# Optimization experiments

Measured on AMD Instinct MI355X. Metric: run time of the kernel, lower is better.

Reference implementation:

```python
import jax, jax.numpy as jnp
import numpy as np


def setup_inputs() -> dict:
    key = jax.random.key(0)
    kx, ky = jax.random.split(key)
    x = jax.random.normal(kx, (4, 8192, 3), dtype=jnp.float32)
    y = jax.random.normal(ky, (4, 8192, 3), dtype=jnp.float32)
    return {"x": x, "y": y}


def _chamfer(x, y):
    # x: [B, N, D], y: [B, M, D]
    x2 = jnp.sum(x * x, axis=-1)                      # [B, N]
    y2 = jnp.sum(y * y, axis=-1)                      # [B, M]
    xy = jnp.einsum("bnd,bmd->bnm", x, y)             # [B, N, M]
    d2 = x2[:, :, None] + y2[:, None, :] - 2.0 * xy   # [B, N, M]
    d2 = jnp.maximum(d2, 0.0)
    cham_x = jnp.min(d2, axis=2).mean(axis=1)         # [B] min over M, mean over N
    cham_y = jnp.min(d2, axis=1).mean(axis=1)         # [B] min over N, mean over M
    return cham_x + cham_y                            # [B]


def reference(x, y):
    per_batch = _chamfer(x, y)
    return jnp.mean(per_batch)  # batch_reduction='mean'
```

## Files before the change

### kernel.cpp

```cpp
#include <hip/hip_runtime.h>


#define N_      8192
#define RPB     4096
#define NRECS   16384
#define NQ      65536
#define FLT_BIG 3.0e38f

typedef float v2f  __attribute__((ext_vector_type(2)));
typedef unsigned int v16u __attribute__((ext_vector_type(16)));

__global__ void zero_out_kernel(float* out) { *out = 0.0f; }

__global__ __launch_bounds__(256) void prep_kernel(
    const float* __restrict__ x, const float* __restrict__ y,
    float4* __restrict__ xrec, float4* __restrict__ yrec,
    unsigned int* __restrict__ pmin, float* __restrict__ out)
{
    int i = blockIdx.x * 256 + threadIdx.x;
    if (i == 0) *out = 0.0f;
    pmin[i]         = 0x7F800000u;
    pmin[i + 32768] = 0x7F800000u;
    int side = i >> 14;
    int r    = i & (NRECS - 1);
    const float* src = side ? y : x;
    float4*      dst = side ? yrec : xrec;
    const float* p = src + (size_t)r * 6;
    float p0x = p[0], p0y = p[1], p0z = p[2];
    float p1x = p[3], p1y = p[4], p1z = p[5];
    float w0 = fmaf(p0x, p0x, fmaf(p0y, p0y, p0z * p0z));
    float w1 = fmaf(p1x, p1x, fmaf(p1y, p1y, p1z * p1z));
    dst[2*r]   = make_float4(p0x, p1x, p0y, p1y);
    dst[2*r+1] = make_float4(p0z, p1z, w0, w1);
}


static __device__ __forceinline__ void s_load2(v16u& a, v16u& b, const unsigned int* p) {
    asm volatile("s_load_dwordx16 %0, %2, 0x0\n\t"
                 "s_load_dwordx16 %1, %2, 0x40"
                 : "=s"(a), "=s"(b) : "s"(p));
}
static __device__ __forceinline__ void s_wait(v16u& a, v16u& b) {
    asm volatile("s_waitcnt lgkmcnt(0)" : "+s"(a), "+s"(b));
}

static __device__ __forceinline__ void do_record(
    const unsigned int* d,
    const v2f* qx, const v2f* qy, const v2f* qz,
    float* acc)
{
    v2f pxs = (v2f){__uint_as_float(d[0]), __uint_as_float(d[1])};
    v2f pys = (v2f){__uint_as_float(d[2]), __uint_as_float(d[3])};
    v2f pzs = (v2f){__uint_as_float(d[4]), __uint_as_float(d[5])};
    v2f w2v = (v2f){__uint_as_float(d[6]), __uint_as_float(d[7])};
    #pragma unroll
    for (int j = 0; j < 4; ++j) {
        v2f td, ts;
        asm("v_pk_fma_f32 %0, %1, %2, %3"
            : "=v"(td) : "v"(qz[j]), "s"(pzs), "v"(w2v));
        asm("v_pk_fma_f32 %0, %1, %2, %3 op_sel:[0,1,1] op_sel_hi:[1,0,0]"
            : "=v"(ts) : "v"(qz[j]), "s"(pzs), "v"(w2v));
        asm("v_pk_fma_f32 %0, %1, %2, %0"
            : "+v"(td) : "v"(qy[j]), "s"(pys));
        asm("v_pk_fma_f32 %0, %1, %2, %0 op_sel:[0,1,0] op_sel_hi:[1,0,1]"
            : "+v"(ts) : "v"(qy[j]), "s"(pys));
        asm("v_pk_fma_f32 %0, %1, %2, %0"
            : "+v"(td) : "v"(qx[j]), "s"(pxs));
        asm("v_pk_fma_f32 %0, %1, %2, %0 op_sel:[0,1,0] op_sel_hi:[1,0,1]"
            : "+v"(ts) : "v"(qx[j]), "s"(pxs));
        asm("v_min3_f32 %0, %0, %1, %2" : "+v"(acc[2*j])   : "v"(td.x), "v"(ts.x));
        asm("v_min3_f32 %0, %0, %1, %2" : "+v"(acc[2*j+1]) : "v"(td.y), "v"(ts.y));
    }
}

__global__ __launch_bounds__(512, 4) void chamfer_kernel(
    const float* __restrict__ xraw, const float* __restrict__ yraw,
    const float4* __restrict__ xrec, const float4* __restrict__ yrec,
    unsigned int* __restrict__ pmin)
{
    __shared__ float red[8 * 512];

    const int tid  = threadIdx.x;
    const int lane = tid & 63;
    const int wave = __builtin_amdgcn_readfirstlane(tid >> 6);
    const int blk  = blockIdx.x;
    const int dir   = blk >> 8;
    const int batch = (blk >> 6) & 3;
    const int qg    = (blk >> 2) & 15;
    const int seg   = blk & 3;

    const float*  qraw = dir ? yraw : xraw;
    const float4* orec = dir ? xrec : yrec;

    const int qbase = batch * N_ + qg * 512;
    float f[24];
    {
        const float4* qv = (const float4*)(qraw + (size_t)qbase * 3) + lane * 6;
        #pragma unroll
        for (int k = 0; k < 6; ++k) {
            float4 t = qv[k];
            f[4*k] = t.x; f[4*k+1] = t.y; f[4*k+2] = t.z; f[4*k+3] = t.w;
        }
    }
    v2f qx[4], qy[4], qz[4];
    float acc[8];
    #pragma unroll
    for (int j = 0; j < 4; ++j) {
        qx[j] = (v2f){-2.0f * f[6*j+0], -2.0f * f[6*j+3]};
        qy[j] = (v2f){-2.0f * f[6*j+1], -2.0f * f[6*j+4]};
        qz[j] = (v2f){-2.0f * f[6*j+2], -2.0f * f[6*j+5]};
        acc[2*j] = FLT_BIG; acc[2*j+1] = FLT_BIG;
    }

    const unsigned int* sp = (const unsigned int*)
        (orec + (size_t)2 * (batch * RPB + seg * 1024 + wave * 128));
    v16u a0, a1, b0, b1;
    s_load2(a0, a1, sp);
    for (int g = 0; g < 32; g += 2) {
        s_wait(a0, a1);
        if (g + 1 < 32) s_load2(b0, b1, sp + (g + 1) * 32);
        {
            unsigned int da[16], db[16];
            #pragma unroll
            for (int t = 0; t < 16; ++t) { da[t] = a0[t]; db[t] = a1[t]; }
            do_record(da,     qx, qy, qz, acc);
            do_record(da + 8, qx, qy, qz, acc);
            do_record(db,     qx, qy, qz, acc);
            do_record(db + 8, qx, qy, qz, acc);
        }
        s_wait(b0, b1);
        if (g + 2 < 32) s_load2(a0, a1, sp + (g + 2) * 32);
        {
            unsigned int da[16], db[16];
            #pragma unroll
            for (int t = 0; t < 16; ++t) { da[t] = b0[t]; db[t] = b1[t]; }
            do_record(da,     qx, qy, qz, acc);
            do_record(da + 8, qx, qy, qz, acc);
            do_record(db,     qx, qy, qz, acc);
            do_record(db + 8, qx, qy, qz, acc);
        }
    }

    #pragma unroll
    for (int j = 0; j < 8; ++j) red[wave * 512 + lane * 8 + j] = acc[j];
    __syncthreads();

    float m = red[tid];
    #pragma unroll
    for (int w = 1; w < 8; ++w) m = fminf(m, red[w * 512 + tid]);
    int gq = qbase + tid;
    float ax = qraw[gq*3+0], ay = qraw[gq*3+1], az = qraw[gq*3+2];
    float qn = fmaf(ax, ax, fmaf(ay, ay, az * az));
    float d2 = fmaxf(0.0f, qn + m);
    atomicMin(&pmin[dir * 32768 + gq], __float_as_uint(d2));
}

__global__ __launch_bounds__(256) void sum_kernel(
    const unsigned int* __restrict__ pmin, float* __restrict__ out)
{
    int i = blockIdx.x * 256 + threadIdx.x;
    float4 v = ((const float4*)pmin)[i];
    float s = v.x + v.y + v.z + v.w;
    #pragma unroll
    for (int off = 32; off > 0; off >>= 1) s += __shfl_xor(s, off);
    if ((threadIdx.x & 63) == 0) atomicAdd(out, s * (1.0f / 32768.0f));
}

__global__ __launch_bounds__(1024) void chamfer_raw_kernel(
    const float* __restrict__ xraw, const float* __restrict__ yraw,
    float* __restrict__ out)
{
    __shared__ float4 red4[16][64];
    const int tid  = threadIdx.x;
    const int wave = tid >> 6;
    const int lane = tid & 63;
    const int blk  = blockIdx.x;
    const bool xdir = (blk < 128);
    const int b    = (blk & 127) >> 5;
    const int qofs = (blk & 31) << 8;
    const float* qraw = xdir ? xraw : yraw;
    const float* oraw = xdir ? yraw : xraw;
    float qx0[4], qx1[4], qx2[4], acc[4];
    #pragma unroll
    for (int q = 0; q < 4; ++q) {
        int gq = b * N_ + qofs + lane*4 + q;
        qx0[q] = qraw[gq*3+0]; qx1[q] = qraw[gq*3+1]; qx2[q] = qraw[gq*3+2];
        acc[q] = FLT_BIG;
    }
    const float* opp = oraw + (size_t)(b * N_ + wave * 512) * 3;
    #pragma unroll 4
    for (int k = 0; k < 512; ++k) {
        float p0 = opp[k*3+0], p1 = opp[k*3+1], p2 = opp[k*3+2];
        float w  = fmaf(p0, p0, fmaf(p1, p1, p2*p2));
        #pragma unroll
        for (int q = 0; q < 4; ++q) {
            float dot = qx0[q]*p0 + qx1[q]*p1 + qx2[q]*p2;
            acc[q] = fminf(acc[q], fmaf(-2.0f, dot, w));
        }
    }
    red4[wave][lane] = make_float4(acc[0], acc[1], acc[2], acc[3]);
    __syncthreads();
    if (tid < 256) {
        const float* red = (const float*)red4;
        float m = red[tid];
        #pragma unroll
        for (int w = 1; w < 16; ++w) m = fminf(m, red[w*256 + tid]);
        int gq = b * N_ + qofs + tid;
        float ax = qraw[gq*3+0], ay = qraw[gq*3+1], az = qraw[gq*3+2];
        float d2 = fmaxf(0.0f, fmaf(ax,ax,fmaf(ay,ay,az*az)) + m);
        #pragma unroll
        for (int off = 32; off > 0; off >>= 1) d2 += __shfl_xor(d2, off);
        if ((tid & 63) == 0) atomicAdd(out, d2 * (1.0f / 32768.0f));
    }
}

extern "C" void kernel_launch(void* const* d_in, const int* in_sizes, int n_in,
                              void* d_out, int out_size, void* d_ws, size_t ws_size,
                              hipStream_t stream)
{
    const float* x = (const float*)d_in[0];
    const float* y = (const float*)d_in[1];
    float* out = (float*)d_out;

    const size_t need = (size_t)NRECS * 2 * 2 * sizeof(float4) + NQ * 4;
    if (ws_size >= need) {
        float4* xrec = (float4*)d_ws;
        float4* yrec = xrec + 2 * NRECS;
        unsigned int* pmin = (unsigned int*)(yrec + 2 * NRECS);
        prep_kernel<<<128, 256, 0, stream>>>(x, y, xrec, yrec, pmin, out);
        chamfer_kernel<<<512, 512, 0, stream>>>(x, y, xrec, yrec, pmin);
        sum_kernel<<<64, 256, 0, stream>>>(pmin, out);
    } else {
        zero_out_kernel<<<1, 1, 0, stream>>>(out);
        chamfer_raw_kernel<<<256, 1024, 0, stream>>>(x, y, out);
    }
}
```

Baseline: 98.04 us.

## Fuse prep and sum into chamfer kernel with LDS records and last-block reduction

Removes the separate prep and sum kernels. Each block now builds its packed opposite-point records, including squared norms, directly in LDS, and reads them from LDS instead of through scalar loads. The cross-segment min goes through a workspace partial buffer plus an atomic counter, and the last-arriving block per group finishes the min and sum. A global counter then writes the final output. This saves launch overhead and global round-trips, but adds a memset, threadfence ordering, and LDS reads in the inner loop, which replace the earlier SGPR operands.

New measurement: 105.6 us. +7.7%, slower.

```diff
diff --git a/kernel.cpp b/kernel.cpp
--- a/kernel.cpp
+++ b/kernel.cpp
@@ -2,72 +2,33 @@
 
 
 #define N_      8192
-#define RPB     4096
-#define NRECS   16384
-#define NQ      65536
+#define NGRP    128
 #define FLT_BIG 3.0e38f
 
-typedef float v2f  __attribute__((ext_vector_type(2)));
-typedef unsigned int v16u __attribute__((ext_vector_type(16)));
+typedef float v2f __attribute__((ext_vector_type(2)));
 
 __global__ void zero_out_kernel(float* out) { *out = 0.0f; }
 
-__global__ __launch_bounds__(256) void prep_kernel(
-    const float* __restrict__ x, const float* __restrict__ y,
-    float4* __restrict__ xrec, float4* __restrict__ yrec,
-    unsigned int* __restrict__ pmin, float* __restrict__ out)
-{
-    int i = blockIdx.x * 256 + threadIdx.x;
-    if (i == 0) *out = 0.0f;
-    pmin[i]         = 0x7F800000u;
-    pmin[i + 32768] = 0x7F800000u;
-    int side = i >> 14;
-    int r    = i & (NRECS - 1);
-    const float* src = side ? y : x;
-    float4*      dst = side ? yrec : xrec;
-    const float* p = src + (size_t)r * 6;
-    float p0x = p[0], p0y = p[1], p0z = p[2];
-    float p1x = p[3], p1y = p[4], p1z = p[5];
-    float w0 = fmaf(p0x, p0x, fmaf(p0y, p0y, p0z * p0z));
-    float w1 = fmaf(p1x, p1x, fmaf(p1y, p1y, p1z * p1z));
-    dst[2*r]   = make_float4(p0x, p1x, p0y, p1y);
-    dst[2*r+1] = make_float4(p0z, p1z, w0, w1);
-}
-
-
-static __device__ __forceinline__ void s_load2(v16u& a, v16u& b, const unsigned int* p) {
-    asm volatile("s_load_dwordx16 %0, %2, 0x0\n\t"
-                 "s_load_dwordx16 %1, %2, 0x40"
-                 : "=s"(a), "=s"(b) : "s"(p));
-}
-static __device__ __forceinline__ void s_wait(v16u& a, v16u& b) {
-    asm volatile("s_waitcnt lgkmcnt(0)" : "+s"(a), "+s"(b));
-}
-
-static __device__ __forceinline__ void do_record(
-    const unsigned int* d,
+static __device__ __forceinline__ void do_record_v(
+    v2f pxs, v2f pys, v2f pzs, v2f wv,
     const v2f* qx, const v2f* qy, const v2f* qz,
     float* acc)
 {
-    v2f pxs = (v2f){__uint_as_float(d[0]), __uint_as_float(d[1])};
-    v2f pys = (v2f){__uint_as_float(d[2]), __uint_as_float(d[3])};
-    v2f pzs = (v2f){__uint_as_float(d[4]), __uint_as_float(d[5])};
-    v2f w2v = (v2f){__uint_as_float(d[6]), __uint_as_float(d[7])};
     #pragma unroll
     for (int j = 0; j < 4; ++j) {
         v2f td, ts;
         asm("v_pk_fma_f32 %0, %1, %2, %3"
-            : "=v"(td) : "v"(qz[j]), "s"(pzs), "v"(w2v));
+            : "=v"(td) : "v"(qz[j]), "v"(pzs), "v"(wv));
         asm("v_pk_fma_f32 %0, %1, %2, %3 op_sel:[0,1,1] op_sel_hi:[1,0,0]"
-            : "=v"(ts) : "v"(qz[j]), "s"(pzs), "v"(w2v));
+            : "=v"(ts) : "v"(qz[j]), "v"(pzs), "v"(wv));
         asm("v_pk_fma_f32 %0, %1, %2, %0"
-            : "+v"(td) : "v"(qy[j]), "s"(pys));
+            : "+v"(td) : "v"(qy[j]), "v"(pys));
         asm("v_pk_fma_f32 %0, %1, %2, %0 op_sel:[0,1,0] op_sel_hi:[1,0,1]"
-            : "+v"(ts) : "v"(qy[j]), "s"(pys));
+            : "+v"(ts) : "v"(qy[j]), "v"(pys));
         asm("v_pk_fma_f32 %0, %1, %2, %0"
-            : "+v"(td) : "v"(qx[j]), "s"(pxs));
+            : "+v"(td) : "v"(qx[j]), "v"(pxs));
         asm("v_pk_fma_f32 %0, %1, %2, %0 op_sel:[0,1,0] op_sel_hi:[1,0,1]"
-            : "+v"(ts) : "v"(qx[j]), "s"(pxs));
+            : "+v"(ts) : "v"(qx[j]), "v"(pxs));
         asm("v_min3_f32 %0, %0, %1, %2" : "+v"(acc[2*j])   : "v"(td.x), "v"(ts.x));
         asm("v_min3_f32 %0, %0, %1, %2" : "+v"(acc[2*j+1]) : "v"(td.y), "v"(ts.y));
     }
@@ -75,10 +36,13 @@
 
 __global__ __launch_bounds__(512, 4) void chamfer_kernel(
     const float* __restrict__ xraw, const float* __restrict__ yraw,
-    const float4* __restrict__ xrec, const float4* __restrict__ yrec,
-    unsigned int* __restrict__ pmin)
-{
-    __shared__ float red[8 * 512];
+    float* __restrict__ partial,
+    unsigned int* __restrict__ ctrl,
+    float* __restrict__ out)
+{
+    __shared__ float4 recs4[2048];
+    __shared__ float  red[8 * 512];
+    __shared__ unsigned int sflag;
 
     const int tid  = threadIdx.x;
     const int lane = tid & 63;
@@ -88,9 +52,25 @@
     const int batch = (blk >> 6) & 3;
     const int qg    = (blk >> 2) & 15;
     const int seg   = blk & 3;
-
-    const float*  qraw = dir ? yraw : xraw;
-    const float4* orec = dir ? xrec : yrec;
+    const int g     = blk >> 2;
+
+    const float* qraw = dir ? yraw : xraw;
+    const float* oraw = dir ? xraw : yraw;
+
+    {
+        const float4* src4 =
+            (const float4*)(oraw + (size_t)(batch * N_ + seg * 2048) * 3) + tid * 3;
+        float4 a = src4[0], b = src4[1], c = src4[2];
+        float w00 = fmaf(a.x, a.x, fmaf(a.y, a.y, a.z * a.z));
+        float w01 = fmaf(a.w, a.w, fmaf(b.x, b.x, b.y * b.y));
+        float w10 = fmaf(b.z, b.z, fmaf(b.w, b.w, c.x * c.x));
+        float w11 = fmaf(c.y, c.y, fmaf(c.z, c.z, c.w * c.w));
+        float4* d = &recs4[tid * 4];
+        d[0] = make_float4(a.x, a.w, a.y, b.x);
+        d[1] = make_float4(a.z, b.y, w00, w01);
+        d[2] = make_float4(b.z, c.y, b.w, c.z);
+        d[3] = make_float4(c.x, c.w, w10, w11);
+    }
 
     const int qbase = batch * N_ + qg * 512;
     float f[24];
@@ -111,59 +91,59 @@
         qz[j] = (v2f){-2.0f * f[6*j+2], -2.0f * f[6*j+5]};
         acc[2*j] = FLT_BIG; acc[2*j+1] = FLT_BIG;
     }
-
-    const unsigned int* sp = (const unsigned int*)
-        (orec + (size_t)2 * (batch * RPB + seg * 1024 + wave * 128));
-    v16u a0, a1, b0, b1;
-    s_load2(a0, a1, sp);
-    for (int g = 0; g < 32; g += 2) {
-        s_wait(a0, a1);
-        if (g + 1 < 32) s_load2(b0, b1, sp + (g + 1) * 32);
-        {
-            unsigned int da[16], db[16];
+    __syncthreads();
+
+    const float* rp = (const float*)&recs4[wave * 256];
+    #pragma unroll 4
+    for (int k = 0; k < 128; ++k) {
+        v2f pxs = *(const v2f*)(rp + k * 8 + 0);
+        v2f pys = *(const v2f*)(rp + k * 8 + 2);
+        v2f pzs = *(const v2f*)(rp + k * 8 + 4);
+        v2f wv  = *(const v2f*)(rp + k * 8 + 6);
+        do_record_v(pxs, pys, pzs, wv, qx, qy, qz, acc);
+    }
+
+    #pragma unroll
+    for (int j = 0; j < 8; ++j) red[wave * 512 + lane * 8 + j] = acc[j];
+    __syncthreads();
+    float m = red[tid];
+    #pragma unroll
+    for (int w = 1; w < 8; ++w) m = fminf(m, red[w * 512 + tid]);
+
+    partial[((size_t)g * 4 + seg) * 512 + tid] = m;
+    __syncthreads();
+    if (tid == 0) {
+        __threadfence();
+        sflag = atomicAdd(&ctrl[g], 1u);
+    }
+    __syncthreads();
+    if (sflag == 3u) {
+        if (tid == 0) __threadfence();
+        __syncthreads();
+        const float* pg = partial + (size_t)g * 4 * 512;
+        float mm = fminf(fminf(pg[tid], pg[512 + tid]),
+                         fminf(pg[1024 + tid], pg[1536 + tid]));
+        int gq = qbase + tid;
+        float ax = qraw[gq*3+0], ay = qraw[gq*3+1], az = qraw[gq*3+2];
+        float qn = fmaf(ax, ax, fmaf(ay, ay, az * az));
+        float d2 = fmaxf(0.0f, qn + mm);
+        #pragma unroll
+        for (int off = 32; off > 0; off >>= 1) d2 += __shfl_xor(d2, off);
+        if (lane == 0) red[wave] = d2;
+        __syncthreads();
+        if (tid == 0) {
+            float s = red[0];
             #pragma unroll
-            for (int t = 0; t < 16; ++t) { da[t] = a0[t]; db[t] = a1[t]; }
-            do_record(da,     qx, qy, qz, acc);
-            do_record(da + 8, qx, qy, qz, acc);
-            do_record(db,     qx, qy, qz, acc);
-            do_record(db + 8, qx, qy, qz, acc);
+            for (int w = 1; w < 8; ++w) s += red[w];
+            atomicAdd((float*)&ctrl[NGRP + 1], s * (1.0f / 32768.0f));
+            __threadfence();
+            unsigned int o2 = atomicAdd(&ctrl[NGRP], 1u);
+            if (o2 == (unsigned)(NGRP - 1)) {
+                float tot = atomicAdd((float*)&ctrl[NGRP + 1], 0.0f);
+                *out = tot;
+            }
         }
-        s_wait(b0, b1);
-        if (g + 2 < 32) s_load2(a0, a1, sp + (g + 2) * 32);
-        {
-            unsigned int da[16], db[16];
-            #pragma unroll
-            for (int t = 0; t < 16; ++t) { da[t] = b0[t]; db[t] = b1[t]; }
-            do_record(da,     qx, qy, qz, acc);
-            do_record(da + 8, qx, qy, qz, acc);
-            do_record(db,     qx, qy, qz, acc);
-            do_record(db + 8, qx, qy, qz, acc);
-        }
-    }
-
-    #pragma unroll
-    for (int j = 0; j < 8; ++j) red[wave * 512 + lane * 8 + j] = acc[j];
-    __syncthreads();
-
-    float m = red[tid];
-    #pragma unroll
-    for (int w = 1; w < 8; ++w) m = fminf(m, red[w * 512 + tid]);
-    int gq = qbase + tid;
-    float ax = qraw[gq*3+0], ay = qraw[gq*3+1], az = qraw[gq*3+2];
-    float qn = fmaf(ax, ax, fmaf(ay, ay, az * az));
-    float d2 = fmaxf(0.0f, qn + m);
-    atomicMin(&pmin[dir * 32768 + gq], __float_as_uint(d2));
-}
-
-__global__ __launch_bounds__(256) void sum_kernel(
-    const unsigned int* __restrict__ pmin, float* __restrict__ out)
-{
-    int i = blockIdx.x * 256 + threadIdx.x;
-    float4 v = ((const float4*)pmin)[i];
-    float s = v.x + v.y + v.z + v.w;
-    #pragma unroll
-    for (int off = 32; off > 0; off >>= 1) s += __shfl_xor(s, off);
-    if ((threadIdx.x & 63) == 0) atomicAdd(out, s * (1.0f / 32768.0f));
+    }
 }
 
 __global__ __launch_bounds__(1024) void chamfer_raw_kernel(
@@ -222,14 +202,12 @@
     const float* y = (const float*)d_in[1];
     float* out = (float*)d_out;
 
-    const size_t need = (size_t)NRECS * 2 * 2 * sizeof(float4) + NQ * 4;
+    const size_t need = (size_t)NGRP * 4 * 512 * sizeof(float) + (NGRP + 2) * 4;
     if (ws_size >= need) {
-        float4* xrec = (float4*)d_ws;
-        float4* yrec = xrec + 2 * NRECS;
-        unsigned int* pmin = (unsigned int*)(yrec + 2 * NRECS);
-        prep_kernel<<<128, 256, 0, stream>>>(x, y, xrec, yrec, pmin, out);
-        chamfer_kernel<<<512, 512, 0, stream>>>(x, y, xrec, yrec, pmin);
-        sum_kernel<<<64, 256, 0, stream>>>(pmin, out);
+        float* partial = (float*)d_ws;
+        unsigned int* ctrl = (unsigned int*)(partial + (size_t)NGRP * 4 * 512);
+        hipMemsetAsync(ctrl, 0, (NGRP + 2) * 4, stream);
+        chamfer_kernel<<<512, 512, 0, stream>>>(x, y, partial, ctrl, out);
     } else {
         zero_out_kernel<<<1, 1, 0, stream>>>(out);
         chamfer_raw_kernel<<<256, 1024, 0, stream>>>(x, y, out);
```

## Split work over 1024 blocks and fuse final reduction via last-block pattern

Applied to the files above, without the earlier changes.

Doubles the number of segments per query group (8 instead of 4) so the chamfer kernel launches 1024 blocks with a higher occupancy hint. Each wave also starts its scalar record loads at a staggered offset. The atomicMin buffer and separate sum kernel are replaced by per-segment partial minima and a last-arriving-block reduction using atomic counters, which also computes the final mean. This removes one kernel launch and the atomicMin traffic, at the cost of a memset, extra partial-buffer writes and reads, and threadfence synchronization.

Measured after the change: 136.7 us. +39.5%, slower.

```diff
diff --git a/kernel.cpp b/kernel.cpp
--- a/kernel.cpp
+++ b/kernel.cpp
@@ -4,7 +4,7 @@
 #define N_      8192
 #define RPB     4096
 #define NRECS   16384
-#define NQ      65536
+#define NGRP    128
 #define FLT_BIG 3.0e38f
 
 typedef float v2f  __attribute__((ext_vector_type(2)));
@@ -14,13 +14,9 @@
 
 __global__ __launch_bounds__(256) void prep_kernel(
     const float* __restrict__ x, const float* __restrict__ y,
-    float4* __restrict__ xrec, float4* __restrict__ yrec,
-    unsigned int* __restrict__ pmin, float* __restrict__ out)
+    float4* __restrict__ xrec, float4* __restrict__ yrec)
 {
     int i = blockIdx.x * 256 + threadIdx.x;
-    if (i == 0) *out = 0.0f;
-    pmin[i]         = 0x7F800000u;
-    pmin[i + 32768] = 0x7F800000u;
     int side = i >> 14;
     int r    = i & (NRECS - 1);
     const float* src = side ? y : x;
@@ -33,7 +29,6 @@
     dst[2*r]   = make_float4(p0x, p1x, p0y, p1y);
     dst[2*r+1] = make_float4(p0z, p1z, w0, w1);
 }
-
 
 static __device__ __forceinline__ void s_load2(v16u& a, v16u& b, const unsigned int* p) {
     asm volatile("s_load_dwordx16 %0, %2, 0x0\n\t"
@@ -73,21 +68,25 @@
     }
 }
 
-__global__ __launch_bounds__(512, 4) void chamfer_kernel(
+__global__ __launch_bounds__(512, 8) void chamfer_kernel(
     const float* __restrict__ xraw, const float* __restrict__ yraw,
     const float4* __restrict__ xrec, const float4* __restrict__ yrec,
-    unsigned int* __restrict__ pmin)
+    float* __restrict__ partial,
+    unsigned int* __restrict__ ctrl,
+    float* __restrict__ out)
 {
     __shared__ float red[8 * 512];
+    __shared__ unsigned int sflag;
 
     const int tid  = threadIdx.x;
     const int lane = tid & 63;
     const int wave = __builtin_amdgcn_readfirstlane(tid >> 6);
     const int blk  = blockIdx.x;
-    const int dir   = blk >> 8;
-    const int batch = (blk >> 6) & 3;
-    const int qg    = (blk >> 2) & 15;
-    const int seg   = blk & 3;
+    const int dir   = blk >> 9;
+    const int batch = (blk >> 7) & 3;
+    const int qg    = (blk >> 3) & 15;
+    const int seg   = blk & 7;
+    const int g     = blk >> 3;
 
     const float*  qraw = dir ? yraw : xraw;
     const float4* orec = dir ? xrec : yrec;
@@ -113,12 +112,13 @@
     }
 
     const unsigned int* sp = (const unsigned int*)
-        (orec + (size_t)2 * (batch * RPB + seg * 1024 + wave * 128));
+        (orec + (size_t)2 * (batch * RPB + seg * 512 + wave * 64));
+    const int off = wave * 2;
     v16u a0, a1, b0, b1;
-    s_load2(a0, a1, sp);
-    for (int g = 0; g < 32; g += 2) {
+    s_load2(a0, a1, sp + ((0 + off) & 15) * 32);
+    for (int i = 0; i < 16; i += 2) {
         s_wait(a0, a1);
-        if (g + 1 < 32) s_load2(b0, b1, sp + (g + 1) * 32);
+        s_load2(b0, b1, sp + (((i + 1) + off) & 15) * 32);
         {
             unsigned int da[16], db[16];
             #pragma unroll
@@ -129,7 +129,7 @@
             do_record(db + 8, qx, qy, qz, acc);
         }
         s_wait(b0, b1);
-        if (g + 2 < 32) s_load2(a0, a1, sp + (g + 2) * 32);
+        if (i + 2 < 16) s_load2(a0, a1, sp + (((i + 2) + off) & 15) * 32);
         {
             unsigned int da[16], db[16];
             #pragma unroll
@@ -144,26 +144,45 @@
     #pragma unroll
     for (int j = 0; j < 8; ++j) red[wave * 512 + lane * 8 + j] = acc[j];
     __syncthreads();
-
     float m = red[tid];
     #pragma unroll
     for (int w = 1; w < 8; ++w) m = fminf(m, red[w * 512 + tid]);
-    int gq = qbase + tid;
-    float ax = qraw[gq*3+0], ay = qraw[gq*3+1], az = qraw[gq*3+2];
-    float qn = fmaf(ax, ax, fmaf(ay, ay, az * az));
-    float d2 = fmaxf(0.0f, qn + m);
-    atomicMin(&pmin[dir * 32768 + gq], __float_as_uint(d2));
-}
-
-__global__ __launch_bounds__(256) void sum_kernel(
-    const unsigned int* __restrict__ pmin, float* __restrict__ out)
-{
-    int i = blockIdx.x * 256 + threadIdx.x;
-    float4 v = ((const float4*)pmin)[i];
-    float s = v.x + v.y + v.z + v.w;
-    #pragma unroll
-    for (int off = 32; off > 0; off >>= 1) s += __shfl_xor(s, off);
-    if ((threadIdx.x & 63) == 0) atomicAdd(out, s * (1.0f / 32768.0f));
+
+    partial[((size_t)g * 8 + seg) * 512 + tid] = m;
+    __syncthreads();
+    if (tid == 0) {
+        __threadfence();
+        sflag = atomicAdd(&ctrl[g], 1u);
+    }
+    __syncthreads();
+    if (sflag == 7u) {
+        if (tid == 0) __threadfence();
+        __syncthreads();
+        const float* pg = partial + (size_t)g * 8 * 512;
+        float mm = pg[tid];
+        #pragma unroll
+        for (int s = 1; s < 8; ++s) mm = fminf(mm, pg[s * 512 + tid]);
+        int gq = qbase + tid;
+        float ax = qraw[gq*3+0], ay = qraw[gq*3+1], az = qraw[gq*3+2];
+        float qn = fmaf(ax, ax, fmaf(ay, ay, az * az));
+        float d2 = fmaxf(0.0f, qn + mm);
+        #pragma unroll
+        for (int o = 32; o > 0; o >>= 1) d2 += __shfl_xor(d2, o);
+        if (lane == 0) red[wave] = d2;
+        __syncthreads();
+        if (tid == 0) {
+            float s = red[0];
+            #pragma unroll
+            for (int w = 1; w < 8; ++w) s += red[w];
+            atomicAdd((float*)&ctrl[NGRP + 1], s * (1.0f / 32768.0f));
+            __threadfence();
+            unsigned int o2 = atomicAdd(&ctrl[NGRP], 1u);
+            if (o2 == (unsigned)(NGRP - 1)) {
+                float tot = atomicAdd((float*)&ctrl[NGRP + 1], 0.0f);
+                *out = tot;
+            }
+        }
+    }
 }
 
 __global__ __launch_bounds__(1024) void chamfer_raw_kernel(
@@ -222,14 +241,17 @@
     const float* y = (const float*)d_in[1];
     float* out = (float*)d_out;
 
-    const size_t need = (size_t)NRECS * 2 * 2 * sizeof(float4) + NQ * 4;
+    const size_t recs_b    = (size_t)NRECS * 2 * 2 * sizeof(float4);
+    const size_t partial_b = (size_t)NGRP * 8 * 512 * sizeof(float);
+    const size_t need = recs_b + partial_b + (NGRP + 2) * 4;
     if (ws_size >= need) {
         float4* xrec = (float4*)d_ws;
         float4* yrec = xrec + 2 * NRECS;
-        unsigned int* pmin = (unsigned int*)(yrec + 2 * NRECS);
-        prep_kernel<<<128, 256, 0, stream>>>(x, y, xrec, yrec, pmin, out);
-        chamfer_kernel<<<512, 512, 0, stream>>>(x, y, xrec, yrec, pmin);
-        sum_kernel<<<64, 256, 0, stream>>>(pmin, out);
+        float*  partial = (float*)(yrec + 2 * NRECS);
+        unsigned int* ctrl = (unsigned int*)(partial + (size_t)NGRP * 8 * 512);
+        hipMemsetAsync(ctrl, 0, (NGRP + 2) * 4, stream);
+        prep_kernel<<<128, 256, 0, stream>>>(x, y, xrec, yrec);
+        chamfer_kernel<<<1024, 512, 0, stream>>>(x, y, xrec, yrec, partial, ctrl, out);
     } else {
         zero_out_kernel<<<1, 1, 0, stream>>>(out);
         chamfer_raw_kernel<<<256, 1024, 0, stream>>>(x, y, out);
```
